# Performance work log

Hardware: AMD Instinct MI355X
Metric: run time of the kernel (lower is better)

The kernel has to match this reference:

```python
import jax, jax.numpy as jnp
import numpy as np

N = 10000
E = 160000
H = 8
C = 128
D = 1024
NB = 3
NG = 64
NEG_SLOPE = 0.2
BN_EPS = 1e-5


def setup_inputs() -> dict:
    key = jax.random.key(0)
    ks = jax.random.split(key, 12)
    x = jax.random.normal(ks[0], (N, D), dtype=jnp.float32)
    edge_index = jax.random.randint(ks[1], (2, E), 0, N, dtype=jnp.int64)
    batch = jnp.sort(jax.random.randint(ks[2], (N,), 0, NG, dtype=jnp.int64))
    W = jax.random.normal(ks[3], (NB, D, D), dtype=jnp.float32) * 0.03
    att_src = jax.random.normal(ks[4], (NB, H, C), dtype=jnp.float32) * 0.1
    att_dst = jax.random.normal(ks[5], (NB, H, C), dtype=jnp.float32) * 0.1
    att_bias = jnp.zeros((NB, D), dtype=jnp.float32)
    gamma = jnp.ones((NB, D), dtype=jnp.float32)
    beta = jnp.zeros((NB, D), dtype=jnp.float32)
    W_out = jax.random.normal(ks[6], (D, 2), dtype=jnp.float32) * 0.03
    b_out = jnp.zeros((2,), dtype=jnp.float32)
    return {"x": x, "edge_index": edge_index, "batch": batch, "W": W,
            "att_src": att_src, "att_dst": att_dst, "att_bias": att_bias,
            "gamma": gamma, "beta": beta, "W_out": W_out, "b_out": b_out}


def _gat_conv(x, Wb, a_src, a_dst, bias, src, dst):
    # linear projection, per-head view: [N, H, C]
    h = (x @ Wb).reshape(N, H, C)
    alpha_src = jnp.einsum('nhc,hc->nh', h, a_src)  # [N,H]
    alpha_dst = jnp.einsum('nhc,hc->nh', h, a_dst)
    e = jax.nn.leaky_relu(alpha_src[src] + alpha_dst[dst], NEG_SLOPE)  # [Etot,H]
    # segment softmax over incoming edges per destination node
    m = jax.ops.segment_max(e, dst, num_segments=N)  # every node has self-loop
    ex = jnp.exp(e - m[dst])
    denom = jax.ops.segment_sum(ex, dst, num_segments=N)
    alpha = ex / denom[dst]  # [Etot,H]
    msg = alpha[:, :, None] * h[src]  # [Etot,H,C]
    out = jax.ops.segment_sum(msg, dst, num_segments=N).reshape(N, H * C)
    return out + bias


def _batchnorm(x, g, b):
    mu = jnp.mean(x, axis=0)
    var = jnp.mean(jnp.square(x - mu), axis=0)  # biased, training mode
    return (x - mu) * jax.lax.rsqrt(var + BN_EPS) * g + b


def reference(x, edge_index, batch, W, att_src, att_dst, att_bias, gamma, beta, W_out, b_out):
    # add self loops (PyG GATConv default)
    loop = jnp.arange(N, dtype=edge_index.dtype)
    src = jnp.concatenate([edge_index[0], loop])
    dst = jnp.concatenate([edge_index[1], loop])

    h = x
    prev = x
    for i in range(NB):
        att = _gat_conv(h, W[i], att_src[i], att_dst[i], att_bias[i], src, dst)
        o = jax.nn.relu(_batchnorm(prev + att, gamma[i], beta[i]))
        prev = h
        h = o

    # global mean pool over graphs
    sums = jax.ops.segment_sum(h, batch, num_segments=NG)
    cnts = jax.ops.segment_sum(jnp.ones((N,), dtype=h.dtype), batch, num_segments=NG)
    pooled = sums / jnp.maximum(cnts, 1.0)[:, None]
    return pooled @ W_out + b_out
```

## Files before the change

kernel.cpp:

```cpp
#include <hip/hip_runtime.h>
#include <hip/hip_bf16.h>

#define N_NODES 10000
#define E_EDGES 160000
#define ETOT    170000
#define H_HEADS 8
#define C_CH    128
#define D_DIM   1024
#define NBLK    3
#define NGRAPH  64
#define NEG_SLOPE 0.2f
#define BN_EPS  1e-5f

typedef __attribute__((ext_vector_type(8))) _Float16 half8;
typedef __attribute__((ext_vector_type(4))) _Float16 half4;
typedef __attribute__((ext_vector_type(2))) _Float16 half2v;
typedef __attribute__((ext_vector_type(4))) float f32x4;

__device__ inline int lower_bound_batch(const int* __restrict__ batch, int g) {
    int lo = 0, hi = N_NODES;
    while (lo < hi) {
        int mid = (lo + hi) >> 1;
        if (batch[mid] < g) lo = mid + 1;
        else hi = mid;
    }
    return lo;
}

__global__ void deg_kernel(const int* __restrict__ ei, int* __restrict__ deg) {
    int tid = blockIdx.x * blockDim.x + threadIdx.x;
    if (tid >= ETOT) return;
    int dst = (tid < E_EDGES) ? ei[E_EDGES + tid] : (tid - E_EDGES);
    atomicAdd(&deg[dst], 1);
}

__global__ void scan_kernel(const int* __restrict__ deg, int* __restrict__ ioff) {
    __shared__ int part[256];
    int t = threadIdx.x;
    const int CH = (N_NODES + 255) / 256;
    int base = t * CH;
    int s = 0;
    for (int j = 0; j < CH; ++j) {
        int idx = base + j;
        if (idx < N_NODES) s += deg[idx];
    }
    part[t] = s;
    __syncthreads();
    for (int o = 1; o < 256; o <<= 1) {
        int v = 0;
        if (t >= o) v = part[t - o];
        __syncthreads();
        part[t] += v;
        __syncthreads();
    }
    int run = (t == 0) ? 0 : part[t - 1];
    for (int j = 0; j < CH; ++j) {
        int idx = base + j;
        if (idx < N_NODES) { ioff[idx] = run; run += deg[idx]; }
    }
}

__global__ void scatter_kernel(const int* __restrict__ ei, int* __restrict__ ioff,
                               int* __restrict__ csr_src, int* __restrict__ csr_dst) {
    int tid = blockIdx.x * blockDim.x + threadIdx.x;
    if (tid >= ETOT) return;
    int src, dst;
    if (tid < E_EDGES) { src = ei[tid]; dst = ei[E_EDGES + tid]; }
    else { src = dst = tid - E_EDGES; }
    int pos = atomicAdd(&ioff[dst], 1);
    csr_src[pos] = src;
    csr_dst[pos] = dst;
}

__global__ __launch_bounds__(256) void xconv_kernel(const float* __restrict__ in,
                                                    _Float16* __restrict__ o, int n4) {
    int i = blockIdx.x * blockDim.x + threadIdx.x;
    if (i >= n4) return;
    float4 v = ((const float4*)in)[i];
    half4 h = {(_Float16)v.x, (_Float16)v.y, (_Float16)v.z, (_Float16)v.w};
    ((half4*)o)[i] = h;
}

__global__ __launch_bounds__(256) void wtconv_kernel(const float* __restrict__ Wall,
                                                     _Float16* __restrict__ t16all) {
    const float* W = Wall + (size_t)blockIdx.z * D_DIM * D_DIM;
    _Float16* t16 = t16all + (size_t)blockIdx.z * D_DIM * D_DIM;
    __shared__ float t[32][33];
    int bn = blockIdx.x * 32;
    int bk = blockIdx.y * 32;
    int tx = threadIdx.x & 31;
    int ty = threadIdx.x >> 5;
#pragma unroll
    for (int r = 0; r < 32; r += 8)
        t[ty + r][tx] = W[(size_t)(bk + ty + r) * D_DIM + bn + tx];
    __syncthreads();
#pragma unroll
    for (int r = 0; r < 32; r += 8)
        t16[(size_t)(bn + ty + r) * D_DIM + bk + tx] = (_Float16)t[tx][ty + r];
}

__global__ __launch_bounds__(256, 4) void gemm_mfma_kernel(const _Float16* __restrict__ A,
                                                           const _Float16* __restrict__ Bt,
                                                           _Float16* __restrict__ Hout,
                                                           const float* __restrict__ att_s,
                                                           const float* __restrict__ att_d,
                                                           float* __restrict__ asrc,
                                                           float* __restrict__ adst,
                                                           float* __restrict__ stats, int M) {
    __shared__ short As[128 * 64];
    __shared__ short Bs[64 * 64];
    int bx = blockIdx.x;
    int tid = threadIdx.x;
    if (bx == 0) {
#pragma unroll
        for (int j = 0; j < 8; ++j) stats[tid + j * 256] = 0.f;
    }
    int c = bx & 7;
    int nt = (bx >> 3) & 15;
    int mt = c + 8 * (bx >> 7);
    if (mt >= 79) return;
    int bm = mt * 128;
    int head = nt >> 1;
    int bncol = (nt & 1) * 64;
    int bnrow = nt * 64;
    int wave = tid >> 6;
    int lane = tid & 63;
    int wm = wave * 32;
    int quad = lane >> 4;
    int l16 = lane & 15;

    f32x4 acc[2][4];
#pragma unroll
    for (int i = 0; i < 2; ++i)
#pragma unroll
        for (int j = 0; j < 4; ++j) acc[i][j] = (f32x4){0.f, 0.f, 0.f, 0.f};

    int srow8 = lane >> 3;
    int sswz = ((lane & 7) ^ srow8) << 4;
    const char* gA[4];
    const char* gB[2];
    char* ldA[4];
    char* ldB[2];
#pragma unroll
    for (int r = 0; r < 4; ++r) {
        int arow = wave * 8 + r * 32 + srow8;
        int ga = bm + arow;
        if (ga > M - 1) ga = M - 1;
        gA[r] = (const char*)(A + (size_t)ga * 1024) + sswz;
        ldA[r] = (char*)As + (wave * 8 + r * 32) * 128;
    }
#pragma unroll
    for (int r = 0; r < 2; ++r) {
        int brow = wave * 8 + r * 32 + srow8;
        gB[r] = (const char*)(Bt + (size_t)(bnrow + brow) * 1024) + sswz;
        ldB[r] = (char*)Bs + (wave * 8 + r * 32) * 128;
    }

    int xr = l16 & 7;
    for (int kb = 0; kb < 16; ++kb) {
        int ko = kb * 128;
#pragma unroll
        for (int r = 0; r < 4; ++r)
            __builtin_amdgcn_global_load_lds(
                (const __attribute__((address_space(1))) void*)(gA[r] + ko),
                (__attribute__((address_space(3))) void*)ldA[r], 16, 0, 0);
#pragma unroll
        for (int r = 0; r < 2; ++r)
            __builtin_amdgcn_global_load_lds(
                (const __attribute__((address_space(1))) void*)(gB[r] + ko),
                (__attribute__((address_space(3))) void*)ldB[r], 16, 0, 0);
        __syncthreads();
#pragma unroll
        for (int h = 0; h < 2; ++h) {
            int sl = (quad + h * 4) ^ xr;
            half8 af[2], bfr[4];
#pragma unroll
            for (int i = 0; i < 2; ++i)
                af[i] = *(const half8*)(As + (wm + i * 16 + l16) * 64 + sl * 8);
#pragma unroll
            for (int j = 0; j < 4; ++j)
                bfr[j] = *(const half8*)(Bs + (j * 16 + l16) * 64 + sl * 8);
#pragma unroll
            for (int i = 0; i < 2; ++i)
#pragma unroll
                for (int j = 0; j < 4; ++j)
                    acc[i][j] = __builtin_amdgcn_mfma_f32_16x16x32_f16(af[i], bfr[j], acc[i][j], 0, 0, 0);
        }
        __syncthreads();
    }

    float wsv[4], wdv[4];
#pragma unroll
    for (int j = 0; j < 4; ++j) {
        int cc = bncol + j * 16 + l16;
        wsv[j] = att_s[head * 128 + cc];
        wdv[j] = att_d[head * 128 + cc];
    }
#pragma unroll
    for (int i = 0; i < 2; ++i) {
#pragma unroll
        for (int reg = 0; reg < 4; ++reg) {
            float p = acc[i][0][reg] * wsv[0] + acc[i][1][reg] * wsv[1] +
                      acc[i][2][reg] * wsv[2] + acc[i][3][reg] * wsv[3];
            float q = acc[i][0][reg] * wdv[0] + acc[i][1][reg] * wdv[1] +
                      acc[i][2][reg] * wdv[2] + acc[i][3][reg] * wdv[3];
#pragma unroll
            for (int o = 1; o < 16; o <<= 1) {
                p += __shfl_xor(p, o);
                q += __shfl_xor(q, o);
            }
            if (l16 == 0) {
                int gr = bm + wm + i * 16 + quad * 4 + reg;
                if (gr < M) {
                    atomicAdd(&asrc[gr * 8 + head], p);
                    atomicAdd(&adst[gr * 8 + head], q);
                }
            }
        }
    }
#pragma unroll
    for (int i = 0; i < 2; ++i) {
#pragma unroll
        for (int reg = 0; reg < 4; ++reg) {
            int gr = bm + wm + i * 16 + quad * 4 + reg;
            if (gr < M) {
                _Float16* hp = Hout + (size_t)head * N_NODES * 128 + (size_t)gr * 128 + bncol + l16;
#pragma unroll
                for (int j = 0; j < 4; ++j) hp[j * 16] = (_Float16)acc[i][j][reg];
            }
        }
    }
}

__global__ __launch_bounds__(256) void edge_exp_kernel(const int* __restrict__ csr_src,
                                                       const int* __restrict__ csr_dst,
                                                       const float* __restrict__ asrc,
                                                       const float* __restrict__ adst,
                                                       float* __restrict__ exw) {
    int p = blockIdx.x * 256 + threadIdx.x;
    if (p >= ETOT) return;
    int s = csr_src[p];
    int d = csr_dst[p];
    float4 s0 = *(const float4*)(asrc + (unsigned)s * 8u);
    float4 s1 = *(const float4*)(asrc + (unsigned)s * 8u + 4u);
    float4 d0 = *(const float4*)(adst + (unsigned)d * 8u);
    float4 d1 = *(const float4*)(adst + (unsigned)d * 8u + 4u);
    float e[8] = {s0.x + d0.x, s0.y + d0.y, s0.z + d0.z, s0.w + d0.w,
                  s1.x + d1.x, s1.y + d1.y, s1.z + d1.z, s1.w + d1.w};
    float4 o0, o1;
#pragma unroll
    for (int j = 0; j < 8; ++j) {
        float v = e[j];
        v = (v > 0.f) ? v : NEG_SLOPE * v;
        float ex = __expf(v);
        if (j < 4) ((float*)&o0)[j] = ex;
        else ((float*)&o1)[j - 4] = ex;
    }
    *(float4*)(exw + (unsigned)p * 8u) = o0;
    *(float4*)(exw + (unsigned)p * 8u + 4u) = o1;
}

__global__ __launch_bounds__(256) void agg_kernel(const _Float16* __restrict__ h16,
                                                  const float* __restrict__ exw,
                                                  const int* __restrict__ ioff,
                                                  const int* __restrict__ csr_src,
                                                  const _Float16* __restrict__ prevh,
                                                  const float* __restrict__ bias,
                                                  _Float16* __restrict__ yout) {
    int bx = blockIdx.x;
    int tid = threadIdx.x;
    int head = bx & 7;
    int chunk = bx >> 3;
    int sub = tid >> 5;
    int lane = tid & 31;
    int n = chunk * 8 + sub;
    unsigned c4 = (unsigned)(lane * 4);
    const _Float16* hh = h16 + (size_t)head * N_NODES * 128;
    const float* exh = exw + head;
    int start = (n == 0) ? 0 : ioff[n - 1];
    int end = ioff[n];
    float den = 0.f;
    float4 acc = make_float4(0.f, 0.f, 0.f, 0.f);
    int p = start;
    for (; p + 4 <= end; p += 4) {
        int s0 = csr_src[p + 0];
        int s1 = csr_src[p + 1];
        int s2 = csr_src[p + 2];
        int s3 = csr_src[p + 3];
        float x0 = exh[(unsigned)p * 8u];
        float x1 = exh[(unsigned)p * 8u + 8u];
        float x2 = exh[(unsigned)p * 8u + 16u];
        float x3 = exh[(unsigned)p * 8u + 24u];
        half4 h0 = *(const half4*)(hh + ((unsigned)s0 * 128u + c4));
        half4 h1 = *(const half4*)(hh + ((unsigned)s1 * 128u + c4));
        half4 h2 = *(const half4*)(hh + ((unsigned)s2 * 128u + c4));
        half4 h3 = *(const half4*)(hh + ((unsigned)s3 * 128u + c4));
        den += (x0 + x1) + (x2 + x3);
        acc.x = fmaf(x0, (float)h0[0], fmaf(x1, (float)h1[0], fmaf(x2, (float)h2[0], fmaf(x3, (float)h3[0], acc.x))));
        acc.y = fmaf(x0, (float)h0[1], fmaf(x1, (float)h1[1], fmaf(x2, (float)h2[1], fmaf(x3, (float)h3[1], acc.y))));
        acc.z = fmaf(x0, (float)h0[2], fmaf(x1, (float)h1[2], fmaf(x2, (float)h2[2], fmaf(x3, (float)h3[2], acc.z))));
        acc.w = fmaf(x0, (float)h0[3], fmaf(x1, (float)h1[3], fmaf(x2, (float)h2[3], fmaf(x3, (float)h3[3], acc.w))));
    }
    for (; p < end; ++p) {
        int s = csr_src[p];
        float x = exh[(unsigned)p * 8u];
        half4 hv = *(const half4*)(hh + ((unsigned)s * 128u + c4));
        den += x;
        acc.x = fmaf(x, (float)hv[0], acc.x);
        acc.y = fmaf(x, (float)hv[1], acc.y);
        acc.z = fmaf(x, (float)hv[2], acc.z);
        acc.w = fmaf(x, (float)hv[3], acc.w);
    }
    float invd = 1.0f / den;
    int col = head * 128 + (int)c4;
    half4 ph = *(const half4*)(prevh + (size_t)n * 1024 + col);
    float4 bv = *(const float4*)(bias + col);
    float r0 = fmaf(acc.x, invd, (float)ph[0] + bv.x);
    float r1 = fmaf(acc.y, invd, (float)ph[1] + bv.y);
    float r2 = fmaf(acc.z, invd, (float)ph[2] + bv.z);
    float r3 = fmaf(acc.w, invd, (float)ph[3] + bv.w);
    half4 o = {(_Float16)r0, (_Float16)r1, (_Float16)r2, (_Float16)r3};
    *(half4*)(yout + (size_t)n * 1024 + col) = o;
}

__global__ void bn_stats_kernel(const _Float16* __restrict__ y, float* __restrict__ stats) {
    int col = (blockIdx.x * 256 + threadIdx.x) * 2;
    float s0 = 0.f, s1 = 0.f, q0 = 0.f, q1 = 0.f;
    for (int r = blockIdx.y; r < N_NODES; r += gridDim.y) {
        half2v v = *(const half2v*)(y + (size_t)r * 1024 + col);
        float a = (float)v[0], b = (float)v[1];
        s0 += a; q0 += a * a;
        s1 += b; q1 += b * b;
    }
    atomicAdd(&stats[col], s0);
    atomicAdd(&stats[col + 1], s1);
    atomicAdd(&stats[1024 + col], q0);
    atomicAdd(&stats[1024 + col + 1], q1);
}

__global__ void bn_apply_kernel(const _Float16* __restrict__ y, const float* __restrict__ stats,
                                const float* __restrict__ gamma, const float* __restrict__ beta,
                                _Float16* __restrict__ oout, float* __restrict__ azero) {
    int idx4 = blockIdx.x * blockDim.x + threadIdx.x;
    if (idx4 < 2 * N_NODES * H_HEADS / 4)
        ((float4*)azero)[idx4] = make_float4(0.f, 0.f, 0.f, 0.f);
    if (idx4 >= N_NODES * D_DIM / 4) return;
    int base = idx4 * 4;
    int col = base & 1023;
    const float invN = 1.0f / (float)N_NODES;
    half4 v = ((const half4*)y)[idx4];
    float r[4];
#pragma unroll
    for (int j = 0; j < 4; ++j) {
        int cc = col + j;
        float mu = stats[cc] * invN;
        float var = stats[1024 + cc] * invN - mu * mu;
        float t = ((float)v[j] - mu) * rsqrtf(var + BN_EPS) * gamma[cc] + beta[cc];
        r[j] = fmaxf(t, 0.f);
    }
    half4 h = {(_Float16)r[0], (_Float16)r[1], (_Float16)r[2], (_Float16)r[3]};
    ((half4*)oout)[idx4] = h;
}

__global__ __launch_bounds__(256) void pool_kernel(const _Float16* __restrict__ h3,
                                                   const int* __restrict__ batch,
                                                   float* __restrict__ pooled) {
    int g = blockIdx.y;
    int col = threadIdx.x * 4;
    int lo = lower_bound_batch(batch, g);
    int hi = lower_bound_batch(batch, g + 1);
    int len = hi - lo;
    int r0 = lo + (int)(((long long)len * blockIdx.x) >> 3);
    int r1 = lo + (int)(((long long)len * (blockIdx.x + 1)) >> 3);
    float a0 = 0.f, a1 = 0.f, a2 = 0.f, a3 = 0.f;
    for (int r = r0; r < r1; ++r) {
        half4 v = *(const half4*)(h3 + (size_t)r * 1024 + col);
        a0 += (float)v[0]; a1 += (float)v[1]; a2 += (float)v[2]; a3 += (float)v[3];
    }
    if (r1 > r0) {
        atomicAdd(&pooled[(size_t)g * 1024 + col + 0], a0);
        atomicAdd(&pooled[(size_t)g * 1024 + col + 1], a1);
        atomicAdd(&pooled[(size_t)g * 1024 + col + 2], a2);
        atomicAdd(&pooled[(size_t)g * 1024 + col + 3], a3);
    }
}

__global__ void final_kernel(const float* __restrict__ pooled, const int* __restrict__ batch,
                             const float* __restrict__ Wout, const float* __restrict__ bout,
                             float* __restrict__ out) {
    int g = blockIdx.x;
    int t = threadIdx.x;
    float p0 = 0.f, p1 = 0.f;
    for (int d = t; d < 1024; d += 256) {
        float v = pooled[(size_t)g * 1024 + d];
        p0 = fmaf(v, Wout[2 * d], p0);
        p1 = fmaf(v, Wout[2 * d + 1], p1);
    }
    __shared__ float s0[256], s1[256];
    s0[t] = p0; s1[t] = p1;
    __syncthreads();
    for (int o = 128; o; o >>= 1) {
        if (t < o) { s0[t] += s0[t + o]; s1[t] += s1[t + o]; }
        __syncthreads();
    }
    if (t == 0) {
        int cnt = lower_bound_batch(batch, g + 1) - lower_bound_batch(batch, g);
        float inv = 1.0f / fmaxf((float)cnt, 1.0f);
        out[g * 2 + 0] = s0[0] * inv + bout[0];
        out[g * 2 + 1] = s1[0] * inv + bout[1];
    }
}

extern "C" void kernel_launch(void* const* d_in, const int* in_sizes, int n_in,
                              void* d_out, int out_size, void* d_ws, size_t ws_size,
                              hipStream_t stream) {
    const float* x        = (const float*)d_in[0];
    const int*   ei       = (const int*)d_in[1];
    const int*   batch    = (const int*)d_in[2];
    const float* W        = (const float*)d_in[3];
    const float* att_src  = (const float*)d_in[4];
    const float* att_dst  = (const float*)d_in[5];
    const float* att_bias = (const float*)d_in[6];
    const float* gamma    = (const float*)d_in[7];
    const float* beta     = (const float*)d_in[8];
    const float* Wout     = (const float*)d_in[9];
    const float* bout     = (const float*)d_in[10];
    float* out = (float*)d_out;

    const size_t ND = (size_t)N_NODES * D_DIM;
    float* ws = (float*)d_ws;
    float* asrc   = ws;
    float* adst   = asrc + (size_t)N_NODES * H_HEADS;
    float* stats  = adst + (size_t)N_NODES * H_HEADS;
    float* pooled = stats + 2 * D_DIM;
    int* ideg     = (int*)(pooled + (size_t)NGRAPH * D_DIM);
    int* ioff     = ideg + N_NODES;
    int* csr_src  = ioff + N_NODES;
    int* csr_dst  = csr_src + ETOT;
    float* exw    = (float*)(csr_dst + ETOT);
    _Float16* bufP  = (_Float16*)(exw + (size_t)ETOT * H_HEADS);
    _Float16* bufO0 = bufP + ND;
    _Float16* h16   = bufO0 + ND;
    _Float16* y16   = h16 + ND;
    _Float16* Wt3   = y16 + ND;

    hipMemsetAsync(ideg, 0, N_NODES * sizeof(int), stream);
    hipMemsetAsync(pooled, 0, (size_t)NGRAPH * D_DIM * sizeof(float), stream);
    hipMemsetAsync(asrc, 0, (size_t)2 * N_NODES * H_HEADS * sizeof(float), stream);
    deg_kernel<<<(ETOT + 255) / 256, 256, 0, stream>>>(ei, ideg);
    scan_kernel<<<1, 256, 0, stream>>>(ideg, ioff);
    scatter_kernel<<<(ETOT + 255) / 256, 256, 0, stream>>>(ei, ioff, csr_src, csr_dst);
    xconv_kernel<<<(int)(ND / 4 + 255) / 256, 256, 0, stream>>>(x, bufP, (int)(ND / 4));
    wtconv_kernel<<<dim3(32, 32, 3), 256, 0, stream>>>(W, Wt3);

    const _Float16* Ain[3]  = {bufP, bufO0, bufP};
    const _Float16* Pin[3]  = {bufP, bufP, bufO0};
    _Float16* Oout[3]       = {bufO0, bufP, bufP};

    for (int i = 0; i < NBLK; ++i) {
        gemm_mfma_kernel<<<1280, 256, 0, stream>>>(
            Ain[i], Wt3 + (size_t)i * D_DIM * D_DIM, h16,
            att_src + i * H_HEADS * C_CH, att_dst + i * H_HEADS * C_CH,
            asrc, adst, stats, N_NODES);
        edge_exp_kernel<<<(ETOT + 255) / 256, 256, 0, stream>>>(csr_src, csr_dst,
                                                                asrc, adst, exw);
        agg_kernel<<<N_NODES, 256, 0, stream>>>(h16, exw, ioff, csr_src,
                                                Pin[i], att_bias + i * D_DIM, y16);
        bn_stats_kernel<<<dim3(2, 128), 256, 0, stream>>>(y16, stats);
        bn_apply_kernel<<<(int)(ND / 4 + 255) / 256, 256, 0, stream>>>(
            y16, stats, gamma + i * D_DIM, beta + i * D_DIM, Oout[i], asrc);
    }

    pool_kernel<<<dim3(8, NGRAPH), 256, 0, stream>>>(bufP, batch, pooled);
    final_kernel<<<NGRAPH, 256, 0, stream>>>(pooled, batch, Wout, bout, out);
}
```

Before: 572.6 us.

## Fuse edge attention exp into aggregation and parallelize edges within each wave

Removes the separate edge_exp kernel and the per-edge exp buffer; the aggregation kernel now computes leaky-relu and exp per edge from asrc/adst directly. Each wave now handles one node for one head, with four edge-parallel subgroups of 16 lanes each covering 8 channels, reduced via cross-lane shuffles. This drops the csr_dst array and the exw write/read traffic and one launch per block. The trade-off is recomputing exp in every channel lane and extra shuffle reductions.

```diff
diff --git a/kernel.cpp b/kernel.cpp
--- a/kernel.cpp
+++ b/kernel.cpp
@@ -61,7 +61,7 @@
 }
 
 __global__ void scatter_kernel(const int* __restrict__ ei, int* __restrict__ ioff,
-                               int* __restrict__ csr_src, int* __restrict__ csr_dst) {
+                               int* __restrict__ csr_src) {
     int tid = blockIdx.x * blockDim.x + threadIdx.x;
     if (tid >= ETOT) return;
     int src, dst;
@@ -69,7 +69,6 @@
     else { src = dst = tid - E_EDGES; }
     int pos = atomicAdd(&ioff[dst], 1);
     csr_src[pos] = src;
-    csr_dst[pos] = dst;
 }
 
 __global__ __launch_bounds__(256) void xconv_kernel(const float* __restrict__ in,
@@ -232,95 +231,66 @@
     }
 }
 
-__global__ __launch_bounds__(256) void edge_exp_kernel(const int* __restrict__ csr_src,
-                                                       const int* __restrict__ csr_dst,
-                                                       const float* __restrict__ asrc,
-                                                       const float* __restrict__ adst,
-                                                       float* __restrict__ exw) {
-    int p = blockIdx.x * 256 + threadIdx.x;
-    if (p >= ETOT) return;
-    int s = csr_src[p];
-    int d = csr_dst[p];
-    float4 s0 = *(const float4*)(asrc + (unsigned)s * 8u);
-    float4 s1 = *(const float4*)(asrc + (unsigned)s * 8u + 4u);
-    float4 d0 = *(const float4*)(adst + (unsigned)d * 8u);
-    float4 d1 = *(const float4*)(adst + (unsigned)d * 8u + 4u);
-    float e[8] = {s0.x + d0.x, s0.y + d0.y, s0.z + d0.z, s0.w + d0.w,
-                  s1.x + d1.x, s1.y + d1.y, s1.z + d1.z, s1.w + d1.w};
-    float4 o0, o1;
-#pragma unroll
-    for (int j = 0; j < 8; ++j) {
-        float v = e[j];
-        v = (v > 0.f) ? v : NEG_SLOPE * v;
-        float ex = __expf(v);
-        if (j < 4) ((float*)&o0)[j] = ex;
-        else ((float*)&o1)[j - 4] = ex;
-    }
-    *(float4*)(exw + (unsigned)p * 8u) = o0;
-    *(float4*)(exw + (unsigned)p * 8u + 4u) = o1;
-}
-
 __global__ __launch_bounds__(256) void agg_kernel(const _Float16* __restrict__ h16,
-                                                  const float* __restrict__ exw,
+                                                  const float* __restrict__ asrc,
+                                                  const float* __restrict__ adst,
                                                   const int* __restrict__ ioff,
                                                   const int* __restrict__ csr_src,
                                                   const _Float16* __restrict__ prevh,
                                                   const float* __restrict__ bias,
                                                   _Float16* __restrict__ yout) {
     int bx = blockIdx.x;
-    int tid = threadIdx.x;
     int head = bx & 7;
-    int chunk = bx >> 3;
-    int sub = tid >> 5;
-    int lane = tid & 31;
-    int n = chunk * 8 + sub;
-    unsigned c4 = (unsigned)(lane * 4);
+    int wave = threadIdx.x >> 6;
+    int lane = threadIdx.x & 63;
+    int sub = lane >> 4;
+    int l16 = lane & 15;
+    unsigned c8 = (unsigned)(l16 * 8);
+    int n = (bx >> 3) * 4 + wave;
     const _Float16* hh = h16 + (size_t)head * N_NODES * 128;
-    const float* exh = exw + head;
     int start = (n == 0) ? 0 : ioff[n - 1];
     int end = ioff[n];
+    float ad = adst[(unsigned)n * 8u + (unsigned)head];
     float den = 0.f;
-    float4 acc = make_float4(0.f, 0.f, 0.f, 0.f);
-    int p = start;
-    for (; p + 4 <= end; p += 4) {
-        int s0 = csr_src[p + 0];
-        int s1 = csr_src[p + 1];
-        int s2 = csr_src[p + 2];
-        int s3 = csr_src[p + 3];
-        float x0 = exh[(unsigned)p * 8u];
-        float x1 = exh[(unsigned)p * 8u + 8u];
-        float x2 = exh[(unsigned)p * 8u + 16u];
-        float x3 = exh[(unsigned)p * 8u + 24u];
-        half4 h0 = *(const half4*)(hh + ((unsigned)s0 * 128u + c4));
-        half4 h1 = *(const half4*)(hh + ((unsigned)s1 * 128u + c4));
-        half4 h2 = *(const half4*)(hh + ((unsigned)s2 * 128u + c4));
-        half4 h3 = *(const half4*)(hh + ((unsigned)s3 * 128u + c4));
-        den += (x0 + x1) + (x2 + x3);
-        acc.x = fmaf(x0, (float)h0[0], fmaf(x1, (float)h1[0], fmaf(x2, (float)h2[0], fmaf(x3, (float)h3[0], acc.x))));
-        acc.y = fmaf(x0, (float)h0[1], fmaf(x1, (float)h1[1], fmaf(x2, (float)h2[1], fmaf(x3, (float)h3[1], acc.y))));
-        acc.z = fmaf(x0, (float)h0[2], fmaf(x1, (float)h1[2], fmaf(x2, (float)h2[2], fmaf(x3, (float)h3[2], acc.z))));
-        acc.w = fmaf(x0, (float)h0[3], fmaf(x1, (float)h1[3], fmaf(x2, (float)h2[3], fmaf(x3, (float)h3[3], acc.w))));
-    }
-    for (; p < end; ++p) {
+    float acc[8];
+#pragma unroll
+    for (int j = 0; j < 8; ++j) acc[j] = 0.f;
+    for (int p = start + sub; p < end; p += 4) {
         int s = csr_src[p];
-        float x = exh[(unsigned)p * 8u];
-        half4 hv = *(const half4*)(hh + ((unsigned)s * 128u + c4));
-        den += x;
-        acc.x = fmaf(x, (float)hv[0], acc.x);
-        acc.y = fmaf(x, (float)hv[1], acc.y);
-        acc.z = fmaf(x, (float)hv[2], acc.z);
-        acc.w = fmaf(x, (float)hv[3], acc.w);
-    }
-    float invd = 1.0f / den;
-    int col = head * 128 + (int)c4;
-    half4 ph = *(const half4*)(prevh + (size_t)n * 1024 + col);
-    float4 bv = *(const float4*)(bias + col);
-    float r0 = fmaf(acc.x, invd, (float)ph[0] + bv.x);
-    float r1 = fmaf(acc.y, invd, (float)ph[1] + bv.y);
-    float r2 = fmaf(acc.z, invd, (float)ph[2] + bv.z);
-    float r3 = fmaf(acc.w, invd, (float)ph[3] + bv.w);
-    half4 o = {(_Float16)r0, (_Float16)r1, (_Float16)r2, (_Float16)r3};
-    *(half4*)(yout + (size_t)n * 1024 + col) = o;
+        float a = asrc[(unsigned)s * 8u + (unsigned)head];
+        half8 hv = *(const half8*)(hh + ((unsigned)s * 128u + c8));
+        float e = a + ad;
+        e = fmaxf(e, NEG_SLOPE * e);
+        float ex = __expf(e);
+        den += ex;
+#pragma unroll
+        for (int j = 0; j < 8; ++j)
+            acc[j] = fmaf(ex, (float)hv[j], acc[j]);
+    }
+#pragma unroll
+    for (int j = 0; j < 8; ++j) {
+        acc[j] += __shfl_xor(acc[j], 16);
+        acc[j] += __shfl_xor(acc[j], 32);
+    }
+    den += __shfl_xor(den, 16);
+    den += __shfl_xor(den, 32);
+    if (sub == 0) {
+        float invd = 1.0f / den;
+        int col = head * 128 + l16 * 8;
+        half8 ph = *(const half8*)(prevh + (size_t)n * 1024 + col);
+        float4 b0 = *(const float4*)(bias + col);
+        float4 b1 = *(const float4*)(bias + col + 4);
+        half8 o;
+        o[0] = (_Float16)fmaf(acc[0], invd, (float)ph[0] + b0.x);
+        o[1] = (_Float16)fmaf(acc[1], invd, (float)ph[1] + b0.y);
+        o[2] = (_Float16)fmaf(acc[2], invd, (float)ph[2] + b0.z);
+        o[3] = (_Float16)fmaf(acc[3], invd, (float)ph[3] + b0.w);
+        o[4] = (_Float16)fmaf(acc[4], invd, (float)ph[4] + b1.x);
+        o[5] = (_Float16)fmaf(acc[5], invd, (float)ph[5] + b1.y);
+        o[6] = (_Float16)fmaf(acc[6], invd, (float)ph[6] + b1.z);
+        o[7] = (_Float16)fmaf(acc[7], invd, (float)ph[7] + b1.w);
+        *(half8*)(yout + (size_t)n * 1024 + col) = o;
+    }
 }
 
 __global__ void bn_stats_kernel(const _Float16* __restrict__ y, float* __restrict__ stats) {
@@ -436,9 +406,7 @@
     int* ideg     = (int*)(pooled + (size_t)NGRAPH * D_DIM);
     int* ioff     = ideg + N_NODES;
     int* csr_src  = ioff + N_NODES;
-    int* csr_dst  = csr_src + ETOT;
-    float* exw    = (float*)(csr_dst + ETOT);
-    _Float16* bufP  = (_Float16*)(exw + (size_t)ETOT * H_HEADS);
+    _Float16* bufP  = (_Float16*)(csr_src + ETOT);
     _Float16* bufO0 = bufP + ND;
     _Float16* h16   = bufO0 + ND;
     _Float16* y16   = h16 + ND;
@@ -449,7 +417,7 @@
     hipMemsetAsync(asrc, 0, (size_t)2 * N_NODES * H_HEADS * sizeof(float), stream);
     deg_kernel<<<(ETOT + 255) / 256, 256, 0, stream>>>(ei, ideg);
     scan_kernel<<<1, 256, 0, stream>>>(ideg, ioff);
-    scatter_kernel<<<(ETOT + 255) / 256, 256, 0, stream>>>(ei, ioff, csr_src, csr_dst);
+    scatter_kernel<<<(ETOT + 255) / 256, 256, 0, stream>>>(ei, ioff, csr_src);
     xconv_kernel<<<(int)(ND / 4 + 255) / 256, 256, 0, stream>>>(x, bufP, (int)(ND / 4));
     wtconv_kernel<<<dim3(32, 32, 3), 256, 0, stream>>>(W, Wt3);
 
@@ -462,10 +430,8 @@
             Ain[i], Wt3 + (size_t)i * D_DIM * D_DIM, h16,
             att_src + i * H_HEADS * C_CH, att_dst + i * H_HEADS * C_CH,
             asrc, adst, stats, N_NODES);
-        edge_exp_kernel<<<(ETOT + 255) / 256, 256, 0, stream>>>(csr_src, csr_dst,
-                                                                asrc, adst, exw);
-        agg_kernel<<<N_NODES, 256, 0, stream>>>(h16, exw, ioff, csr_src,
-                                                Pin[i], att_bias + i * D_DIM, y16);
+        agg_kernel<<<(N_NODES / 4) * H_HEADS, 256, 0, stream>>>(
+            h16, asrc, adst, ioff, csr_src, Pin[i], att_bias + i * D_DIM, y16);
         bn_stats_kernel<<<dim3(2, 128), 256, 0, stream>>>(y16, stats);
         bn_apply_kernel<<<(int)(ND / 4 + 255) / 256, 256, 0, stream>>>(
             y16, stats, gamma + i * D_DIM, beta + i * D_DIM, Oout[i], asrc);
```

Measured after the change: 593.7 us. 1.04x slower.
